# Optimization experiments

Measured on AMD Instinct MI355X. Metric: run time of the kernel, lower is better.

## Reference

```python
import jax, jax.numpy as jnp
import numpy as np

N = 50000
LEAKY_SLOPE = 0.2


def gat_layer(x, src, dst, W, a_src, a_dst, bias, concat):
    """PyG-style GATConv (eval mode, self-loops already in src/dst).
    x: [N, Fin]; W: [Fin, H*C]; a_src, a_dst: [H, C]; bias: [H*C] or [C].
    """
    H, C = a_src.shape
    h = (x @ W).reshape(-1, H, C)                      # [N, H, C]
    alpha_src = jnp.einsum('nhc,hc->nh', h, a_src)      # [N, H]
    alpha_dst = jnp.einsum('nhc,hc->nh', h, a_dst)      # [N, H]
    e = jax.nn.leaky_relu(alpha_src[src] + alpha_dst[dst], LEAKY_SLOPE)  # [E, H]
    # scatter-softmax over incoming edges of each destination node
    m = jax.lax.stop_gradient(jax.ops.segment_max(e, dst, num_segments=N))
    e = jnp.exp(e - m[dst])
    denom = jax.ops.segment_sum(e, dst, num_segments=N)  # [N, H]
    alpha = e / (denom[dst] + 1e-16)                     # [E, H]
    msg = h[src] * alpha[:, :, None]                     # [E, H, C]
    out = jax.ops.segment_sum(msg, dst, num_segments=N)  # [N, H, C]
    out = out.reshape(-1, H * C) if concat else out.mean(axis=1)
    return out + bias


def setup_inputs() -> dict:
    key = jax.random.key(0)
    ks = jax.random.split(key, 10)
    Fin, Hd, Hh = 256, 64, 4
    E = 1600000
    x = jax.random.normal(ks[0], (N, Fin), dtype=jnp.float32)
    edge_index = jax.random.randint(ks[1], (2, E), 0, N, dtype=jnp.int64)
    s = 1.0 / np.sqrt(Fin)
    W1 = jax.random.normal(ks[2], (Fin, Hh * Hd), dtype=jnp.float32) * s
    att_src1 = jax.random.normal(ks[3], (Hh, Hd), dtype=jnp.float32) * (1.0 / np.sqrt(Hd))
    att_dst1 = jax.random.normal(ks[4], (Hh, Hd), dtype=jnp.float32) * (1.0 / np.sqrt(Hd))
    b1 = jnp.zeros((Hh * Hd,), dtype=jnp.float32)
    W2 = jax.random.normal(ks[5], (Hh * Hd, Hd), dtype=jnp.float32) * (1.0 / np.sqrt(Hh * Hd))
    att_src2 = jax.random.normal(ks[6], (1, Hd), dtype=jnp.float32) * (1.0 / np.sqrt(Hd))
    att_dst2 = jax.random.normal(ks[7], (1, Hd), dtype=jnp.float32) * (1.0 / np.sqrt(Hd))
    b2 = jnp.zeros((Hd,), dtype=jnp.float32)
    return {"x": x, "edge_index": edge_index, "W1": W1, "att_src1": att_src1,
            "att_dst1": att_dst1, "b1": b1, "W2": W2, "att_src2": att_src2,
            "att_dst2": att_dst2, "b2": b2}


def reference(x, edge_index, W1, att_src1, att_dst1, b1, W2, att_src2, att_dst2, b2):
    # PyG GATConv adds self-loops by default
    loop = jnp.arange(N, dtype=edge_index.dtype)
    src = jnp.concatenate([edge_index[0], loop])
    dst = jnp.concatenate([edge_index[1], loop])
    h = gat_layer(x, src, dst, W1, att_src1, att_dst1, b1, concat=True)
    h = jax.nn.elu(h)            # dropout is identity in eval mode
    out = gat_layer(h, src, dst, W2, att_src2, att_dst2, b2, concat=False)
    return out
```

## Files before the change

### kernel.cpp

```cpp
#include <hip/hip_runtime.h>


typedef __attribute__((ext_vector_type(8))) short short8;
typedef __attribute__((ext_vector_type(4))) float floatx4;
typedef __attribute__((ext_vector_type(2))) float fx2;

#define FIN 256
#define H1 4
#define CH 64
#define CAP 16384

__device__ __forceinline__ float bf2f(ushort u) {
    union { unsigned int i; float f; } v; v.i = ((unsigned int)u) << 16; return v.f;
}
__device__ __forceinline__ ushort f2bf(float f) {
    union { float f; unsigned int i; } v; v.f = f;
    unsigned int r = v.i + 0x7fffu + ((v.i >> 16) & 1u);
    return (ushort)(r >> 16);
}
__device__ __forceinline__ float load_in(const void* p, int i, int f) {
    return f ? ((const float*)p)[i] : bf2f(((const ushort*)p)[i]);
}
__device__ __forceinline__ int load_idx(const void* p, long long i, int f64) {
    return f64 ? (int)((const long long*)p)[i] : ((const int*)p)[i];
}

__device__ __forceinline__ int pk_off(int row, int k, int KT) {
    return (((row >> 4) * KT + (k >> 5)) << 9) + (((k >> 3) & 3) << 7) +
           ((row & 15) << 3) + (k & 7);
}
__device__ __forceinline__ void pk_dec(int po0, int& row, int& k) {
    int tile = po0 >> 9;
    row = ((tile >> 3) << 4) + ((po0 >> 3) & 15);
    k = ((tile & 7) << 5) + (((po0 >> 7) & 3) << 3);
}

__device__ __forceinline__ float edge_p(float s) {
    s = fmaxf(s, 0.2f * s);
    return __expf(s);
}

__device__ __forceinline__ void accum16(fx2* acc, uint4 v0, uint4 v1,
                                        float p, float& l) {
    l += p;
    fx2 pv = {p, p};
    unsigned w[8] = {v0.x, v0.y, v0.z, v0.w, v1.x, v1.y, v1.z, v1.w};
#pragma unroll
    for (int u = 0; u < 8; ++u) {
        union { unsigned i; float fl; } lo, hi;
        lo.i = w[u] << 16; hi.i = w[u] & 0xffff0000u;
        fx2 c = {lo.fl, hi.fl};
        acc[u] += pv * c;
    }
}

__device__ __forceinline__ void accum8(fx2* acc, uint4 v, float p, float& l) {
    l += p;
    fx2 pv = {p, p};
    unsigned w[4] = {v.x, v.y, v.z, v.w};
#pragma unroll
    for (int u = 0; u < 4; ++u) {
        union { unsigned i; float fl; } lo, hi;
        lo.i = w[u] << 16; hi.i = w[u] & 0xffff0000u;
        fx2 c = {lo.fl, hi.fl};
        acc[u] += pv * c;
    }
}

__global__ __launch_bounds__(256) void probe_kernel(const ushort* __restrict__ x,
                                                    const int* __restrict__ ei,
                                                    int* __restrict__ flags,
                                                    int* __restrict__ bcnt) {
    __shared__ int s_nan, s_odd;
    int t = threadIdx.x;
    bcnt[t] = 0;
    if (t == 0) { s_nan = 0; s_odd = 0; }
    __syncthreads();
    int nanc = 0, oddc = 0;
    for (int i = t; i < 16384; i += 256) {
        ushort u = x[i];
        if (((u >> 7) & 0xFF) == 0xFF) nanc++;
    }
    for (int i = t; i < 2048; i += 256)
        if (ei[2 * i + 1] != 0) oddc++;
    if (nanc) atomicAdd(&s_nan, nanc);
    if (oddc) atomicAdd(&s_odd, oddc);
    __syncthreads();
    if (t == 0) {
        flags[0] = (s_nan >= 2) ? 1 : 0;
        flags[1] = (s_odd == 0) ? 1 : 0;
    }
}

__global__ __launch_bounds__(256) void prep_bucket_kernel(
        const void* __restrict__ x, const void* __restrict__ W1,
        const void* __restrict__ W2, ushort* __restrict__ xb,
        ushort* __restrict__ Wt1, ushort* __restrict__ Wt2,
        const void* __restrict__ ei, int* __restrict__ bcnt,
        unsigned int* __restrict__ buckets,
        int E, int Etot, int Nn, const int* __restrict__ flags,
        int PB_conv, int PB_tr_end) {
    __shared__ int lcnt[256], lbase[256], lcur[256];
    int bid = blockIdx.x, t = threadIdx.x;
    int f = flags[0];
    if (bid < PB_conv) {
        int po0 = bid * 2048 + t * 8;
        int row, k0; pk_dec(po0, row, k0);
        int si = row * FIN + k0;
        if (f) {
            float4 v0 = ((const float4*)x)[si / 4];
            float4 v1 = ((const float4*)x)[si / 4 + 1];
            ushort4 o0, o1;
            o0.x = f2bf(v0.x); o0.y = f2bf(v0.y); o0.z = f2bf(v0.z); o0.w = f2bf(v0.w);
            o1.x = f2bf(v1.x); o1.y = f2bf(v1.y); o1.z = f2bf(v1.z); o1.w = f2bf(v1.w);
            *(ushort4*)(xb + po0) = o0;
            *(ushort4*)(xb + po0 + 4) = o1;
        } else {
            *(uint4*)(xb + po0) = ((const uint4*)x)[si / 8];
        }
        return;
    }
    if (bid < PB_tr_end) {
        int j = (bid - PB_conv) * 256 + t;
        if (j < (FIN * FIN) / 8) {
            int po0 = j * 8;
            int n, k0; pk_dec(po0, n, k0);
            ushort4 o0, o1;
            o0.x = f2bf(load_in(W1, (k0 + 0) * FIN + n, f));
            o0.y = f2bf(load_in(W1, (k0 + 1) * FIN + n, f));
            o0.z = f2bf(load_in(W1, (k0 + 2) * FIN + n, f));
            o0.w = f2bf(load_in(W1, (k0 + 3) * FIN + n, f));
            o1.x = f2bf(load_in(W1, (k0 + 4) * FIN + n, f));
            o1.y = f2bf(load_in(W1, (k0 + 5) * FIN + n, f));
            o1.z = f2bf(load_in(W1, (k0 + 6) * FIN + n, f));
            o1.w = f2bf(load_in(W1, (k0 + 7) * FIN + n, f));
            *(ushort4*)(Wt1 + po0) = o0;
            *(ushort4*)(Wt1 + po0 + 4) = o1;
        } else {
            int po0 = (j - (FIN * FIN) / 8) * 8;
            int n, k0; pk_dec(po0, n, k0);
            ushort4 o0, o1;
            o0.x = f2bf(load_in(W2, (k0 + 0) * CH + n, f));
            o0.y = f2bf(load_in(W2, (k0 + 1) * CH + n, f));
            o0.z = f2bf(load_in(W2, (k0 + 2) * CH + n, f));
            o0.w = f2bf(load_in(W2, (k0 + 3) * CH + n, f));
            o1.x = f2bf(load_in(W2, (k0 + 4) * CH + n, f));
            o1.y = f2bf(load_in(W2, (k0 + 5) * CH + n, f));
            o1.z = f2bf(load_in(W2, (k0 + 6) * CH + n, f));
            o1.w = f2bf(load_in(W2, (k0 + 7) * CH + n, f));
            *(ushort4*)(Wt2 + po0) = o0;
            *(ushort4*)(Wt2 + po0 + 4) = o1;
        }
        return;
    }
    lcnt[t] = 0; lcur[t] = 0;
    __syncthreads();
    int f64 = flags[1];
    int base = (bid - PB_tr_end) * 4096 + t;
    unsigned int val[16]; int bk[16]; bool ok[16];
#pragma unroll
    for (int j = 0; j < 16; ++j) {
        int e = base + j * 256;
        ok[j] = e < Etot;
        bk[j] = 0; val[j] = 0;
        if (ok[j]) {
            int s, d;
            if (e < E) {
                s = load_idx(ei, e, f64);
                d = load_idx(ei, (long long)E + e, f64);
            } else {
                s = d = e - E;
            }
            s = min(max(s, 0), Nn - 1);
            d = min(max(d, 0), Nn - 1);
            bk[j] = d >> 8;
            val[j] = ((unsigned int)s << 8) | (unsigned int)(d & 255);
            atomicAdd(&lcnt[bk[j]], 1);
        }
    }
    __syncthreads();
    if (lcnt[t] > 0) lbase[t] = atomicAdd(&bcnt[t], lcnt[t]);
    __syncthreads();
#pragma unroll
    for (int j = 0; j < 16; ++j) {
        if (ok[j]) {
            int p = lbase[bk[j]] + atomicAdd(&lcur[bk[j]], 1);
            if (p < CAP) buckets[(size_t)bk[j] * CAP + p] = val[j];
        }
    }
}

__device__ __forceinline__ void gemm_core(const ushort* __restrict__ A,
                                          const ushort* __restrict__ Bt,
                                          ushort* __restrict__ C,
                                          int M, int Nc,
                                          const void* __restrict__ aS,
                                          const void* __restrict__ aD,
                                          float* __restrict__ alphaS,
                                          float* __restrict__ alphaD,
                                          int H, int f, int gx, int head,
                                          int planar) {
    const int KT = FIN >> 5;
    int tid = threadIdx.x;
    int wave = tid >> 6, lane = tid & 63, quad = lane >> 4, l16 = lane & 15;
    int rbase = gx * 256 + wave * 64;
    int cbase = head * 64;
    int lsub = (quad << 7) + (l16 << 3);
    floatx4 acc[4][4];
#pragma unroll
    for (int i = 0; i < 4; i++)
#pragma unroll
        for (int j = 0; j < 4; j++) acc[i][j] = (floatx4)0.f;

#pragma unroll 2
    for (int kb = 0; kb < FIN; kb += 32) {
        int kt = kb >> 5;
        short8 a[4], b[4];
#pragma unroll
        for (int mt = 0; mt < 4; mt++) {
            int tr = (rbase + mt * 16) >> 4;
            a[mt] = *reinterpret_cast<const short8*>(
                A + (((size_t)(tr * KT + kt)) << 9) + lsub);
        }
#pragma unroll
        for (int nt = 0; nt < 4; nt++) {
            int tc = (cbase + nt * 16) >> 4;
            b[nt] = *reinterpret_cast<const short8*>(
                Bt + (((size_t)(tc * KT + kt)) << 9) + lsub);
        }
#pragma unroll
        for (int mt = 0; mt < 4; mt++)
#pragma unroll
            for (int nt = 0; nt < 4; nt++)
                acc[mt][nt] = __builtin_amdgcn_mfma_f32_16x16x32_bf16(
                    a[mt], b[nt], acc[mt][nt], 0, 0, 0);
    }
    float asv[4], adv[4];
#pragma unroll
    for (int nt = 0; nt < 4; nt++) {
        int col = cbase + nt * 16 + l16;
        asv[nt] = load_in(aS, col, f);
        adv[nt] = load_in(aD, col, f);
    }
#pragma unroll
    for (int mt = 0; mt < 4; mt++) {
#pragma unroll
        for (int r = 0; r < 4; r++) {
            int row = rbase + mt * 16 + quad * 4 + r;
            float ps = 0.f, pd = 0.f;
#pragma unroll
            for (int nt = 0; nt < 4; nt++) {
                float w = acc[mt][nt][r];
                ps += w * asv[nt];
                pd += w * adv[nt];
            }
#pragma unroll
            for (int off = 8; off > 0; off >>= 1) {
                ps += __shfl_xor(ps, off, 16);
                pd += __shfl_xor(pd, off, 16);
            }
            if (row < M) {
                if (l16 == 0) {
                    alphaS[row * H + head] = ps;
                    alphaD[row * H + head] = pd;
                }
#pragma unroll
                for (int nt = 0; nt < 4; nt++) {
                    int col = cbase + nt * 16 + l16;
                    size_t caddr = planar
                        ? ((size_t)(col >> 7) * M + row) * 128 + (col & 127)
                        : (size_t)row * Nc + col;
                    C[caddr] = f2bf(acc[mt][nt][r]);
                }
            }
        }
    }
}

__global__ __launch_bounds__(256) void gemm1_pass2_kernel(
        const ushort* __restrict__ A, const ushort* __restrict__ Bt,
        ushort* __restrict__ C, int M, int Nc,
        const void* __restrict__ aS, const void* __restrict__ aD,
        float* __restrict__ alphaS, float* __restrict__ alphaD,
        const int* __restrict__ flags, int g1, int nbx,
        const int* __restrict__ bcnt, const unsigned int* __restrict__ buckets,
        int* __restrict__ offs, int* __restrict__ csr_src, int Nn) {
    __shared__ int part[256], sc[256], cur[256];
    int bid = blockIdx.x;
    int t = threadIdx.x;
    if (bid < g1) {
        gemm_core(A, Bt, C, M, Nc, aS, aD, alphaS, alphaD, 4, flags[0],
                  bid % nbx, bid / nbx, 1);
        return;
    }
    int b = bid - g1;
    part[t] = bcnt[t];
    __syncthreads();
#pragma unroll
    for (int off = 1; off < 256; off <<= 1) {
        int v = (t >= off) ? part[t - off] : 0;
        __syncthreads();
        part[t] += v;
        __syncthreads();
    }
    int basepos = (b == 0) ? 0 : part[b - 1];
    int nEdges = min(bcnt[b], CAP);
    sc[t] = 0;
    __syncthreads();
    const unsigned int* bk = buckets + (size_t)b * CAP;
    for (int i = t; i < nEdges; i += 256)
        atomicAdd(&sc[bk[i] & 255], 1);
    __syncthreads();
    int mycount = sc[t];
    __syncthreads();
#pragma unroll
    for (int off = 1; off < 256; off <<= 1) {
        int v = (t >= off) ? sc[t - off] : 0;
        __syncthreads();
        sc[t] += v;
        __syncthreads();
    }
    int excl = sc[t] - mycount;
    int gnode = b * 256 + t;
    if (gnode <= Nn) offs[gnode] = basepos + excl;
    cur[t] = excl;
    __syncthreads();
    for (int i = t; i < nEdges; i += 256) {
        unsigned int v = bk[i];
        int p = atomicAdd(&cur[v & 255], 1);
        csr_src[basepos + p] = (int)(v >> 8);
    }
}

__global__ __launch_bounds__(256) void gemm2_kernel(const ushort* __restrict__ A,
                                                    const ushort* __restrict__ Bt,
                                                    ushort* __restrict__ C,
                                                    int M, int Nc,
                                                    const void* __restrict__ aS,
                                                    const void* __restrict__ aD,
                                                    float* __restrict__ alphaS,
                                                    float* __restrict__ alphaD,
                                                    const int* __restrict__ flags) {
    gemm_core(A, Bt, C, M, Nc, aS, aD, alphaS, alphaD, 1, flags[0],
              blockIdx.x, blockIdx.y, 0);
}

__global__ __launch_bounds__(256) void gat_node1_pass(
        const int* __restrict__ csr_src, const int* __restrict__ offs,
        const float* __restrict__ asrc, const float* __restrict__ adst,
        const ushort* __restrict__ h1p, const void* __restrict__ b1,
        ushort* __restrict__ hmidb, int Nn, const int* __restrict__ flags,
        int plane) {
    int f = flags[0];
    int wave = threadIdx.x >> 6, lane = threadIdx.x & 63;
    int n = blockIdx.x * 4 + wave;
    if (n >= Nn) return;
    int slot = lane >> 3, cg = lane & 7;
    int head = plane * 2 + (cg >> 2);
    float ad = adst[n * H1 + head];
    unsigned rowbase = (unsigned)(plane * Nn) * 128u + (unsigned)cg * 16u;
    int beg = offs[n], end = offs[n + 1];
    fx2 acc[8];
#pragma unroll
    for (int u = 0; u < 8; ++u) acc[u] = (fx2)0.f;
    float l = 0.f;

    int e = beg;
    while (e + 32 <= end) {
        int sj[4]; uint4 v0[4], v1[4]; float pj[4];
#pragma unroll
        for (int j = 0; j < 4; ++j) sj[j] = csr_src[e + 8 * j + slot];
#pragma unroll
        for (int j = 0; j < 4; ++j) {
            const uint4* r = (const uint4*)(h1p + rowbase + (unsigned)sj[j] * 128u);
            v0[j] = r[0]; v1[j] = r[1];
        }
#pragma unroll
        for (int j = 0; j < 4; ++j) pj[j] = edge_p(asrc[sj[j] * H1 + head] + ad);
#pragma unroll
        for (int j = 0; j < 4; ++j) accum16(acc, v0[j], v1[j], pj[j], l);
        e += 32;
    }
    if (e + 16 <= end) {
        int sa = csr_src[e + slot];
        int sb = csr_src[e + 8 + slot];
        const uint4* ra = (const uint4*)(h1p + rowbase + (unsigned)sa * 128u);
        const uint4* rb = (const uint4*)(h1p + rowbase + (unsigned)sb * 128u);
        uint4 va0 = ra[0], va1 = ra[1];
        uint4 vb0 = rb[0], vb1 = rb[1];
        float pa = edge_p(asrc[sa * H1 + head] + ad);
        float pb = edge_p(asrc[sb * H1 + head] + ad);
        accum16(acc, va0, va1, pa, l);
        accum16(acc, vb0, vb1, pb, l);
        e += 16;
    }
    if (e < end) {
        int ea = e + slot, eb = e + 8 + slot;
        bool oka = ea < end, okb = eb < end;
        int sa = csr_src[oka ? ea : beg];
        int sb = csr_src[okb ? eb : beg];
        const uint4* ra = (const uint4*)(h1p + rowbase + (unsigned)sa * 128u);
        const uint4* rb = (const uint4*)(h1p + rowbase + (unsigned)sb * 128u);
        uint4 va0 = ra[0], va1 = ra[1];
        uint4 vb0 = rb[0], vb1 = rb[1];
        float pa = edge_p(oka ? asrc[sa * H1 + head] + ad : -1e30f);
        float pb = edge_p(okb ? asrc[sb * H1 + head] + ad : -1e30f);
        accum16(acc, va0, va1, pa, l);
        accum16(acc, vb0, vb1, pb, l);
    }
#pragma unroll
    for (int off = 8; off <= 32; off <<= 1) {
#pragma unroll
        for (int u = 0; u < 8; ++u) {
            acc[u][0] += __shfl_xor(acc[u][0], off);
            acc[u][1] += __shfl_xor(acc[u][1], off);
        }
        l += __shfl_xor(l, off);
    }
    if (slot == 0) {
        float inv = 1.f / (l + 1e-16f);
        int cb = plane * 128 + cg * 16;
        unsigned ow[8];
#pragma unroll
        for (int u = 0; u < 8; ++u) {
            float o0 = acc[u][0] * inv + load_in(b1, cb + 2 * u, f);
            float o1 = acc[u][1] * inv + load_in(b1, cb + 2 * u + 1, f);
            o0 = o0 > 0.f ? o0 : __expf(o0) - 1.f;
            o1 = o1 > 0.f ? o1 : __expf(o1) - 1.f;
            ow[u] = (unsigned)f2bf(o0) | ((unsigned)f2bf(o1) << 16);
        }
        uint4 st0, st1;
        st0.x = ow[0]; st0.y = ow[1]; st0.z = ow[2]; st0.w = ow[3];
        st1.x = ow[4]; st1.y = ow[5]; st1.z = ow[6]; st1.w = ow[7];
        int po0 = pk_off(n, cb, FIN >> 5);
        int po1 = pk_off(n, cb + 8, FIN >> 5);
        *(uint4*)(hmidb + po0) = st0;
        *(uint4*)(hmidb + po1) = st1;
    }
}

__global__ __launch_bounds__(256) void gat_node2(const int* __restrict__ csr_src,
                                                 const int* __restrict__ offs,
                                                 const float* __restrict__ asrc,
                                                 const float* __restrict__ adst,
                                                 const ushort* __restrict__ h2b,
                                                 const void* __restrict__ b2,
                                                 void* __restrict__ out, int Nn,
                                                 const int* __restrict__ flags) {
    int f = flags[0];
    int wave = threadIdx.x >> 6, lane = threadIdx.x & 63;
    int n = blockIdx.x * 4 + wave;
    if (n >= Nn) return;
    int slot = lane >> 3, cg = lane & 7;
    float ad = adst[n];
    unsigned rowoff = (unsigned)cg * 8u;
    int beg = offs[n], end = offs[n + 1];
    fx2 acc[4];
#pragma unroll
    for (int u = 0; u < 4; ++u) acc[u] = (fx2)0.f;
    float l = 0.f;

    int e = beg;
    while (e + 32 <= end) {
        int sj[4]; uint4 vj[4]; float pj[4];
#pragma unroll
        for (int j = 0; j < 4; ++j) sj[j] = csr_src[e + 8 * j + slot];
#pragma unroll
        for (int j = 0; j < 4; ++j)
            vj[j] = *(const uint4*)(h2b + rowoff + (unsigned)sj[j] * 64u);
#pragma unroll
        for (int j = 0; j < 4; ++j) pj[j] = edge_p(asrc[sj[j]] + ad);
#pragma unroll
        for (int j = 0; j < 4; ++j) accum8(acc, vj[j], pj[j], l);
        e += 32;
    }
    if (e + 16 <= end) {
        int sa = csr_src[e + slot];
        int sb = csr_src[e + 8 + slot];
        uint4 va = *(const uint4*)(h2b + rowoff + (unsigned)sa * 64u);
        uint4 vb = *(const uint4*)(h2b + rowoff + (unsigned)sb * 64u);
        float pa = edge_p(asrc[sa] + ad);
        float pb = edge_p(asrc[sb] + ad);
        accum8(acc, va, pa, l);
        accum8(acc, vb, pb, l);
        e += 16;
    }
    if (e < end) {
        int ea = e + slot, eb = e + 8 + slot;
        bool oka = ea < end, okb = eb < end;
        int sa = csr_src[oka ? ea : beg];
        int sb = csr_src[okb ? eb : beg];
        uint4 va = *(const uint4*)(h2b + rowoff + (unsigned)sa * 64u);
        uint4 vb = *(const uint4*)(h2b + rowoff + (unsigned)sb * 64u);
        float pa = edge_p(oka ? asrc[sa] + ad : -1e30f);
        float pb = edge_p(okb ? asrc[sb] + ad : -1e30f);
        accum8(acc, va, pa, l);
        accum8(acc, vb, pb, l);
    }
#pragma unroll
    for (int off = 8; off <= 32; off <<= 1) {
#pragma unroll
        for (int u = 0; u < 4; ++u) {
            acc[u][0] += __shfl_xor(acc[u][0], off);
            acc[u][1] += __shfl_xor(acc[u][1], off);
        }
        l += __shfl_xor(l, off);
    }
    if (slot == 0) {
        float inv = 1.f / (l + 1e-16f);
        float o[8];
#pragma unroll
        for (int u = 0; u < 4; ++u) {
            o[2 * u]     = acc[u][0] * inv + load_in(b2, cg * 8 + 2 * u, f);
            o[2 * u + 1] = acc[u][1] * inv + load_in(b2, cg * 8 + 2 * u + 1, f);
        }
        if (f) {
            float* op = (float*)out + (unsigned)n * 64u + (unsigned)cg * 8u;
            float4 s0, s1;
            s0.x = o[0]; s0.y = o[1]; s0.z = o[2]; s0.w = o[3];
            s1.x = o[4]; s1.y = o[5]; s1.z = o[6]; s1.w = o[7];
            *(float4*)op = s0;
            *(float4*)(op + 4) = s1;
        } else {
            uint4 st;
            st.x = (unsigned)f2bf(o[0]) | ((unsigned)f2bf(o[1]) << 16);
            st.y = (unsigned)f2bf(o[2]) | ((unsigned)f2bf(o[3]) << 16);
            st.z = (unsigned)f2bf(o[4]) | ((unsigned)f2bf(o[5]) << 16);
            st.w = (unsigned)f2bf(o[6]) | ((unsigned)f2bf(o[7]) << 16);
            *(uint4*)((ushort*)out + (unsigned)n * 64u + (unsigned)cg * 8u) = st;
        }
    }
}

extern "C" void kernel_launch(void* const* d_in, const int* in_sizes, int n_in,
                              void* d_out, int out_size, void* d_ws, size_t ws_size,
                              hipStream_t stream) {
    const void* x   = d_in[0];
    const void* ei  = d_in[1];
    const void* W1  = d_in[2];
    const void* as1 = d_in[3];
    const void* ad1 = d_in[4];
    const void* b1  = d_in[5];
    const void* W2  = d_in[6];
    const void* as2 = d_in[7];
    const void* ad2 = d_in[8];
    const void* b2  = d_in[9];

    const int Nn = in_sizes[0] / FIN;
    const int E  = in_sizes[1] / 2;
    const int ET = E + Nn;
    const int NB = (Nn + 255) >> 8;

    char* ws = (char*)d_ws;
    size_t off = 0;
    auto alloc = [&](size_t bytes) {
        size_t o = off;
        off += (bytes + 255) & ~(size_t)255;
        return o;
    };
    ushort* xb    = (ushort*)(ws + alloc((size_t)Nn * FIN * 2));
    ushort* h1b   = (ushort*)(ws + alloc((size_t)Nn * FIN * 2));
    ushort* hmidb = (ushort*)(ws + alloc((size_t)Nn * FIN * 2));
    ushort* h2b   = (ushort*)(ws + alloc((size_t)Nn * CH * 2));
    ushort* Wt1   = (ushort*)(ws + alloc((size_t)FIN * FIN * 2));
    ushort* Wt2   = (ushort*)(ws + alloc((size_t)CH * FIN * 2));
    float* as1f   = (float*)(ws + alloc((size_t)Nn * H1 * 4));
    float* ad1f   = (float*)(ws + alloc((size_t)Nn * H1 * 4));
    float* as2f   = (float*)(ws + alloc((size_t)Nn * 4));
    float* ad2f   = (float*)(ws + alloc((size_t)Nn * 4));
    int*   offs   = (int*)(ws + alloc((size_t)(Nn + 1) * 4));
    int*   csr    = (int*)(ws + alloc((size_t)ET * 4));
    unsigned int* buckets = (unsigned int*)(ws + alloc((size_t)256 * CAP * 4));
    int*   bcnt   = (int*)(ws + alloc(256 * 4));
    int*   flags  = (int*)(ws + alloc(256));
    (void)ws_size; (void)n_in; (void)out_size;

    probe_kernel<<<1, 256, 0, stream>>>((const ushort*)x, (const int*)ei, flags, bcnt);

    int PB_conv = (Nn * FIN) / 2048;
    int PB_tr   = (FIN * FIN + CH * FIN) / 2048;
    int PB_bkt  = (ET + 4095) / 4096;
    prep_bucket_kernel<<<PB_conv + PB_tr + PB_bkt, 256, 0, stream>>>(
        x, W1, W2, xb, Wt1, Wt2, ei, bcnt, buckets,
        E, ET, Nn, flags, PB_conv, PB_conv + PB_tr);

    int nbx = (Nn + 255) / 256;
    int g1 = nbx * H1;
    gemm1_pass2_kernel<<<g1 + NB, 256, 0, stream>>>(
        xb, Wt1, h1b, Nn, FIN, as1, ad1, as1f, ad1f,
        flags, g1, nbx, bcnt, buckets, offs, csr, Nn);

    gat_node1_pass<<<(Nn + 3) / 4, 256, 0, stream>>>(
        csr, offs, as1f, ad1f, h1b, b1, hmidb, Nn, flags, 0);
    gat_node1_pass<<<(Nn + 3) / 4, 256, 0, stream>>>(
        csr, offs, as1f, ad1f, h1b, b1, hmidb, Nn, flags, 1);

    gemm2_kernel<<<dim3((Nn + 255) / 256, 1), 256, 0, stream>>>(
        hmidb, Wt2, h2b, Nn, CH, as2, ad2, as2f, ad2f, flags);
    gat_node2<<<(Nn + 3) / 4, 256, 0, stream>>>(csr, offs, as2f, ad2f, h2b, b2, d_out, Nn, flags);
}
```

Measured before the change: 384.7 us.

## Reorder CSR blocks first, per-wave LDS histograms, row-major hmid, drop 32-edge unroll

```diff
diff --git a/kernel.cpp b/kernel.cpp
--- a/kernel.cpp
+++ b/kernel.cpp
@@ -199,7 +199,7 @@
                                           float* __restrict__ alphaS,
                                           float* __restrict__ alphaD,
                                           int H, int f, int gx, int head,
-                                          int planar) {
+                                          int planar, int packedA) {
     const int KT = FIN >> 5;
     int tid = threadIdx.x;
     int wave = tid >> 6, lane = tid & 63, quad = lane >> 4, l16 = lane & 15;
@@ -218,9 +218,16 @@
         short8 a[4], b[4];
 #pragma unroll
         for (int mt = 0; mt < 4; mt++) {
-            int tr = (rbase + mt * 16) >> 4;
-            a[mt] = *reinterpret_cast<const short8*>(
-                A + (((size_t)(tr * KT + kt)) << 9) + lsub);
+            if (packedA) {
+                int tr = (rbase + mt * 16) >> 4;
+                a[mt] = *reinterpret_cast<const short8*>(
+                    A + (((size_t)(tr * KT + kt)) << 9) + lsub);
+            } else {
+                int row = rbase + mt * 16 + l16;
+                if (row >= M) row = M - 1;
+                a[mt] = *reinterpret_cast<const short8*>(
+                    A + (size_t)row * FIN + kb + quad * 8);
+            }
         }
 #pragma unroll
         for (int nt = 0; nt < 4; nt++) {
@@ -282,19 +289,22 @@
         ushort* __restrict__ C, int M, int Nc,
         const void* __restrict__ aS, const void* __restrict__ aD,
         float* __restrict__ alphaS, float* __restrict__ alphaD,
-        const int* __restrict__ flags, int g1, int nbx,
+        const int* __restrict__ flags, int NB, int nbx,
         const int* __restrict__ bcnt, const unsigned int* __restrict__ buckets,
         int* __restrict__ offs, int* __restrict__ csr_src, int Nn) {
-    __shared__ int part[256], sc[256], cur[256];
+    __shared__ int part[256], sc[256], sc4[4][256];
     int bid = blockIdx.x;
     int t = threadIdx.x;
-    if (bid < g1) {
+    if (bid >= NB) {
+        int g = bid - NB;
         gemm_core(A, Bt, C, M, Nc, aS, aD, alphaS, alphaD, 4, flags[0],
-                  bid % nbx, bid / nbx, 1);
+                  g % nbx, g / nbx, 1, 1);
         return;
     }
-    int b = bid - g1;
+    int b = bid;
+    int w = t >> 6;
     part[t] = bcnt[t];
+    sc4[0][t] = 0; sc4[1][t] = 0; sc4[2][t] = 0; sc4[3][t] = 0;
     __syncthreads();
 #pragma unroll
     for (int off = 1; off < 256; off <<= 1) {
@@ -305,13 +315,13 @@
     }
     int basepos = (b == 0) ? 0 : part[b - 1];
     int nEdges = min(bcnt[b], CAP);
-    sc[t] = 0;
-    __syncthreads();
     const unsigned int* bk = buckets + (size_t)b * CAP;
     for (int i = t; i < nEdges; i += 256)
-        atomicAdd(&sc[bk[i] & 255], 1);
-    __syncthreads();
-    int mycount = sc[t];
+        atomicAdd(&sc4[w][bk[i] & 255], 1);
+    __syncthreads();
+    int c0 = sc4[0][t], c1 = sc4[1][t], c2 = sc4[2][t], c3 = sc4[3][t];
+    int mycount = c0 + c1 + c2 + c3;
+    sc[t] = mycount;
     __syncthreads();
 #pragma unroll
     for (int off = 1; off < 256; off <<= 1) {
@@ -323,11 +333,14 @@
     int excl = sc[t] - mycount;
     int gnode = b * 256 + t;
     if (gnode <= Nn) offs[gnode] = basepos + excl;
-    cur[t] = excl;
+    sc4[0][t] = excl;
+    sc4[1][t] = excl + c0;
+    sc4[2][t] = excl + c0 + c1;
+    sc4[3][t] = excl + c0 + c1 + c2;
     __syncthreads();
     for (int i = t; i < nEdges; i += 256) {
         unsigned int v = bk[i];
-        int p = atomicAdd(&cur[v & 255], 1);
+        int p = atomicAdd(&sc4[w][v & 255], 1);
         csr_src[basepos + p] = (int)(v >> 8);
     }
 }
@@ -342,7 +355,7 @@
                                                     float* __restrict__ alphaD,
                                                     const int* __restrict__ flags) {
     gemm_core(A, Bt, C, M, Nc, aS, aD, alphaS, alphaD, 1, flags[0],
-              blockIdx.x, blockIdx.y, 0);
+              blockIdx.x, blockIdx.y, 0, 0);
 }
 
 __global__ __launch_bounds__(256) void gat_node1_pass(
@@ -366,30 +379,17 @@
     float l = 0.f;
 
     int e = beg;
-    while (e + 32 <= end) {
-        int sj[4]; uint4 v0[4], v1[4]; float pj[4];
-#pragma unroll
-        for (int j = 0; j < 4; ++j) sj[j] = csr_src[e + 8 * j + slot];
-#pragma unroll
-        for (int j = 0; j < 4; ++j) {
-            const uint4* r = (const uint4*)(h1p + rowbase + (unsigned)sj[j] * 128u);
-            v0[j] = r[0]; v1[j] = r[1];
-        }
-#pragma unroll
-        for (int j = 0; j < 4; ++j) pj[j] = edge_p(asrc[sj[j] * H1 + head] + ad);
-#pragma unroll
-        for (int j = 0; j < 4; ++j) accum16(acc, v0[j], v1[j], pj[j], l);
-        e += 32;
-    }
-    if (e + 16 <= end) {
+    while (e + 16 <= end) {
         int sa = csr_src[e + slot];
         int sb = csr_src[e + 8 + slot];
+        float aa = asrc[sa * H1 + head];
+        float ab = asrc[sb * H1 + head];
         const uint4* ra = (const uint4*)(h1p + rowbase + (unsigned)sa * 128u);
         const uint4* rb = (const uint4*)(h1p + rowbase + (unsigned)sb * 128u);
         uint4 va0 = ra[0], va1 = ra[1];
         uint4 vb0 = rb[0], vb1 = rb[1];
-        float pa = edge_p(asrc[sa * H1 + head] + ad);
-        float pb = edge_p(asrc[sb * H1 + head] + ad);
+        float pa = edge_p(aa + ad);
+        float pb = edge_p(ab + ad);
         accum16(acc, va0, va1, pa, l);
         accum16(acc, vb0, vb1, pb, l);
         e += 16;
@@ -399,12 +399,14 @@
         bool oka = ea < end, okb = eb < end;
         int sa = csr_src[oka ? ea : beg];
         int sb = csr_src[okb ? eb : beg];
+        float aa = asrc[sa * H1 + head];
+        float ab = asrc[sb * H1 + head];
         const uint4* ra = (const uint4*)(h1p + rowbase + (unsigned)sa * 128u);
         const uint4* rb = (const uint4*)(h1p + rowbase + (unsigned)sb * 128u);
         uint4 va0 = ra[0], va1 = ra[1];
         uint4 vb0 = rb[0], vb1 = rb[1];
-        float pa = edge_p(oka ? asrc[sa * H1 + head] + ad : -1e30f);
-        float pb = edge_p(okb ? asrc[sb * H1 + head] + ad : -1e30f);
+        float pa = edge_p(oka ? aa + ad : -1e30f);
+        float pb = edge_p(okb ? ab + ad : -1e30f);
         accum16(acc, va0, va1, pa, l);
         accum16(acc, vb0, vb1, pb, l);
     }
@@ -432,10 +434,8 @@
         uint4 st0, st1;
         st0.x = ow[0]; st0.y = ow[1]; st0.z = ow[2]; st0.w = ow[3];
         st1.x = ow[4]; st1.y = ow[5]; st1.z = ow[6]; st1.w = ow[7];
-        int po0 = pk_off(n, cb, FIN >> 5);
-        int po1 = pk_off(n, cb + 8, FIN >> 5);
-        *(uint4*)(hmidb + po0) = st0;
-        *(uint4*)(hmidb + po1) = st1;
+        uint4* dst = (uint4*)(hmidb + (size_t)n * 256 + cb);
+        dst[0] = st0; dst[1] = st1;
     }
 }
 
@@ -461,26 +461,15 @@
     float l = 0.f;
 
     int e = beg;
-    while (e + 32 <= end) {
-        int sj[4]; uint4 vj[4]; float pj[4];
-#pragma unroll
-        for (int j = 0; j < 4; ++j) sj[j] = csr_src[e + 8 * j + slot];
-#pragma unroll
-        for (int j = 0; j < 4; ++j)
-            vj[j] = *(const uint4*)(h2b + rowoff + (unsigned)sj[j] * 64u);
-#pragma unroll
-        for (int j = 0; j < 4; ++j) pj[j] = edge_p(asrc[sj[j]] + ad);
-#pragma unroll
-        for (int j = 0; j < 4; ++j) accum8(acc, vj[j], pj[j], l);
-        e += 32;
-    }
-    if (e + 16 <= end) {
+    while (e + 16 <= end) {
         int sa = csr_src[e + slot];
         int sb = csr_src[e + 8 + slot];
+        float aa = asrc[sa];
+        float ab = asrc[sb];
         uint4 va = *(const uint4*)(h2b + rowoff + (unsigned)sa * 64u);
         uint4 vb = *(const uint4*)(h2b + rowoff + (unsigned)sb * 64u);
-        float pa = edge_p(asrc[sa] + ad);
-        float pb = edge_p(asrc[sb] + ad);
+        float pa = edge_p(aa + ad);
+        float pb = edge_p(ab + ad);
         accum8(acc, va, pa, l);
         accum8(acc, vb, pb, l);
         e += 16;
@@ -490,10 +479,12 @@
         bool oka = ea < end, okb = eb < end;
         int sa = csr_src[oka ? ea : beg];
         int sb = csr_src[okb ? eb : beg];
+        float aa = asrc[sa];
+        float ab = asrc[sb];
         uint4 va = *(const uint4*)(h2b + rowoff + (unsigned)sa * 64u);
         uint4 vb = *(const uint4*)(h2b + rowoff + (unsigned)sb * 64u);
-        float pa = edge_p(oka ? asrc[sa] + ad : -1e30f);
-        float pb = edge_p(okb ? asrc[sb] + ad : -1e30f);
+        float pa = edge_p(oka ? aa + ad : -1e30f);
+        float pb = edge_p(okb ? ab + ad : -1e30f);
         accum8(acc, va, pa, l);
         accum8(acc, vb, pb, l);
     }
@@ -586,9 +577,9 @@
 
     int nbx = (Nn + 255) / 256;
     int g1 = nbx * H1;
-    gemm1_pass2_kernel<<<g1 + NB, 256, 0, stream>>>(
+    gemm1_pass2_kernel<<<NB + g1, 256, 0, stream>>>(
         xb, Wt1, h1b, Nn, FIN, as1, ad1, as1f, ad1f,
-        flags, g1, nbx, bcnt, buckets, offs, csr, Nn);
+        flags, NB, nbx, bcnt, buckets, offs, csr, Nn);
 
     gat_node1_pass<<<(Nn + 3) / 4, 256, 0, stream>>>(
         csr, offs, as1f, ad1f, h1b, b1, hmidb, Nn, flags, 0);
```

Result: faster. 354.5 us (-7.8%).
